# Optimization experiments

Hardware: AMD Instinct MI355X
Metric: run time of the kernel (lower is better)

Reference implementation:

```python
import jax, jax.numpy as jnp
import numpy as np

B, T, C = 2, 2048, 1024
NH = 16
DFF = 4096
EPS = 1e-5


def setup_inputs() -> dict:
    key = jax.random.key(0)
    ks = jax.random.split(key, 12)
    s = 0.02
    return {
        "x": jax.random.normal(ks[0], (B, T, C), dtype=jnp.float32),
        "Wq": jax.random.normal(ks[1], (C, C), dtype=jnp.float32) * s,
        "bq": jax.random.normal(ks[2], (C,), dtype=jnp.float32) * s,
        "Wk": jax.random.normal(ks[3], (C, C), dtype=jnp.float32) * s,
        "bk": jax.random.normal(ks[4], (C,), dtype=jnp.float32) * s,
        "Wv": jax.random.normal(ks[5], (C, C), dtype=jnp.float32) * s,
        "bv": jax.random.normal(ks[6], (C,), dtype=jnp.float32) * s,
        "W1": jax.random.normal(ks[7], (C, DFF), dtype=jnp.float32) * s,
        "b1": jax.random.normal(ks[8], (DFF,), dtype=jnp.float32) * s,
        "W2": jax.random.normal(ks[9], (DFF, C), dtype=jnp.float32) * s,
        "b2": jax.random.normal(ks[10], (C,), dtype=jnp.float32) * s,
        "ln_w": jnp.ones((C,), dtype=jnp.float32),
    }


def _layernorm(x, w):
    # LayerNorm over last dim, weight only (bias=False), eps=1e-5
    mu = jnp.mean(x, axis=-1, keepdims=True)
    var = jnp.mean(jnp.square(x - mu), axis=-1, keepdims=True)
    return (x - mu) / jnp.sqrt(var + EPS) * w


def reference(x, Wq, bq, Wk, bk, Wv, bv, W1, b1, W2, b2, ln_w):
    Bx, Tx, Cx = x.shape
    hd = Cx // NH
    q = (x @ Wq + bq).reshape(Bx, Tx, NH, hd).transpose(0, 2, 1, 3)  # [B,H,T,hd]
    k = (x @ Wk + bk).reshape(Bx, Tx, NH, hd).transpose(0, 2, 1, 3)
    v = (x @ Wv + bv).reshape(Bx, Tx, NH, hd).transpose(0, 2, 1, 3)
    # NOTE: original scales by sqrt(d_k) = sqrt(FULL model dim C), not head dim
    scores = jnp.einsum("bhqd,bhkd->bhqk", q, k) / jnp.sqrt(jnp.float32(Cx))
    causal = jnp.tril(jnp.ones((Tx, Tx), dtype=bool))
    scores = jnp.where(causal[None, None, :, :], scores, -jnp.inf)
    attn = jax.nn.softmax(scores, axis=-1)
    head_out = jnp.einsum("bhqk,bhkd->bhqd", attn, v)
    a = head_out.transpose(0, 2, 1, 3).reshape(Bx, Tx, Cx)
    # residuals: out = x + ln(x) with SHARED ln weight
    h = a + _layernorm(a, ln_w)
    f = jax.nn.relu(h @ W1 + b1) @ W2 + b2
    out = f + _layernorm(f, ln_w)
    return out
```

## Files before the change

kernel.cpp:

```cpp
#include <hip/hip_runtime.h>
#include <math.h>


typedef __attribute__((ext_vector_type(8))) short short8;
typedef __attribute__((ext_vector_type(4))) float f32x4;

__device__ __forceinline__ unsigned short f2bf(float f) {
    unsigned u = __builtin_bit_cast(unsigned, f);
    unsigned r = u + 0x7fffu + ((u >> 16) & 1u);
    return (unsigned short)(r >> 16);
}

__global__ __launch_bounds__(256) void prep_kernel(
    const float* __restrict__ x,  const float* __restrict__ Wq,
    const float* __restrict__ Wk, const float* __restrict__ Wv,
    const float* __restrict__ W1, const float* __restrict__ W2,
    const float* __restrict__ bq, const float* __restrict__ bk,
    unsigned short* __restrict__ x_bf,  unsigned short* __restrict__ Wqk_t,
    unsigned short* __restrict__ Wvt,   unsigned short* __restrict__ W1t,
    unsigned short* __restrict__ W2t,   float* __restrict__ bqk)
{
    const int bid = blockIdx.x;
    const int tid = threadIdx.x;

    if (bid < 4096) {
        const int i = (bid * 256 + tid) * 4;
        float4 v = *(const float4*)(x + i);
        ushort4 o;
        o.x = f2bf(v.x); o.y = f2bf(v.y); o.z = f2bf(v.z); o.w = f2bf(v.w);
        *(ushort4*)(x_bf + i) = o;
        return;
    }
    if (bid >= 6912) {
        const int i = (bid - 6912) * 256 + tid;
        bqk[i] = i < 1024 ? bq[i] : bk[i - 1024];
        return;
    }

    __shared__ float tile[64][65];
    const float* src; unsigned short* dst; int K, N, t;
    if (bid < 4352)      { t = bid - 4096; src = Wq; dst = Wqk_t;           K = 1024; N = 1024; }
    else if (bid < 4608) { t = bid - 4352; src = Wk; dst = Wqk_t + 1048576; K = 1024; N = 1024; }
    else if (bid < 4864) { t = bid - 4608; src = Wv; dst = Wvt;             K = 1024; N = 1024; }
    else if (bid < 5888) { t = bid - 4864; src = W1; dst = W1t;             K = 1024; N = 4096; }
    else                 { t = bid - 5888; src = W2; dst = W2t;             K = 4096; N = 1024; }

    const int ncols = N >> 6;
    const int n0 = (t % ncols) * 64;
    const int k0 = (t / ncols) * 64;
    const int tx = tid & 15;
    const int ty = tid >> 4;
#pragma unroll
    for (int i = 0; i < 4; ++i) {
        const int r = ty + i * 16;
        float4 v = *(const float4*)(src + (size_t)(k0 + r) * N + n0 + tx * 4);
        tile[r][tx * 4 + 0] = v.x;
        tile[r][tx * 4 + 1] = v.y;
        tile[r][tx * 4 + 2] = v.z;
        tile[r][tx * 4 + 3] = v.w;
    }
    __syncthreads();
#pragma unroll
    for (int i = 0; i < 4; ++i) {
        const int n = ty + i * 16;
        ushort4 o;
        o.x = f2bf(tile[tx * 4 + 0][n]);
        o.y = f2bf(tile[tx * 4 + 1][n]);
        o.z = f2bf(tile[tx * 4 + 2][n]);
        o.w = f2bf(tile[tx * 4 + 3][n]);
        *(ushort4*)(dst + (size_t)(n0 + n) * K + k0 + tx * 4) = o;
    }
}

template <int TM, int TN>
__device__ __forceinline__ void gemm_body(
    unsigned short* As, unsigned short* Bs,
    const unsigned short* __restrict__ A, const unsigned short* __restrict__ Bt,
    const float* __restrict__ bias, float* __restrict__ Cf,
    unsigned short* __restrict__ Cb, int M, int N, int K, int mode,
    int bx, int by, int kbeg, int kend)
{
    constexpr int NI   = TM / 32;
    constexpr int NJ   = TN / 32;
    constexpr int NPA  = TM / 8;
    constexpr int NPB  = TN / 8;
    constexpr int MAXA = (NPA + 3) / 4;
    constexpr int MAXB = (NPB + 3) / 4;

    const int tid  = threadIdx.x;
    const int lane = tid & 63;
    const int w    = tid >> 6;
    const int wm   = (w & 1) * (TM / 2);
    const int wn   = (w >> 1) * (TN / 2);
    const int fm   = lane & 15;
    const int quad = lane >> 4;

    const int row0 = by * TM;
    const int col0 = bx * TN;

    const int srow = lane >> 3;
    const int scol = ((lane & 7) ^ srow) << 3;

    const unsigned short* aptr[MAXA];
    int aoff[MAXA];
#pragma unroll
    for (int i = 0; i < MAXA; ++i) {
        const int p = w + i * 4;
        if (p < NPA) {
            aptr[i] = A + (size_t)(row0 + p * 8 + srow) * K + scol;
            aoff[i] = p * 8 * 64;
        }
    }
    const unsigned short* bptr[MAXB];
    int boff[MAXB];
#pragma unroll
    for (int i = 0; i < MAXB; ++i) {
        const int p = w + i * 4;
        if (p < NPB) {
            bptr[i] = Bt + (size_t)(col0 + p * 8 + srow) * K + scol;
            boff[i] = p * 8 * 64;
        }
    }

    f32x4 acc[NI][NJ] = {};

    for (int k0 = kbeg; k0 < kend; k0 += 64) {
        __syncthreads();
#pragma unroll
        for (int i = 0; i < MAXA; ++i)
            if (w + i * 4 < NPA)
                __builtin_amdgcn_global_load_lds(
                    (const __attribute__((address_space(1))) void*)(aptr[i] + k0),
                    (__attribute__((address_space(3))) void*)&As[aoff[i]], 16, 0, 0);
#pragma unroll
        for (int i = 0; i < MAXB; ++i)
            if (w + i * 4 < NPB)
                __builtin_amdgcn_global_load_lds(
                    (const __attribute__((address_space(1))) void*)(bptr[i] + k0),
                    (__attribute__((address_space(3))) void*)&Bs[boff[i]], 16, 0, 0);
        __syncthreads();

#pragma unroll
        for (int kh = 0; kh < 2; ++kh) {
            short8 af[NI], bf[NJ];
#pragma unroll
            for (int i = 0; i < NI; ++i) {
                const int r = wm + i * 16 + fm;
                const int sl = ((kh << 2) | quad) ^ (r & 7);
                af[i] = *(const short8*)&As[r * 64 + sl * 8];
            }
#pragma unroll
            for (int j = 0; j < NJ; ++j) {
                const int r = wn + j * 16 + fm;
                const int sl = ((kh << 2) | quad) ^ (r & 7);
                bf[j] = *(const short8*)&Bs[r * 64 + sl * 8];
            }
#pragma unroll
            for (int i = 0; i < NI; ++i)
#pragma unroll
                for (int j = 0; j < NJ; ++j)
                    acc[i][j] = __builtin_amdgcn_mfma_f32_16x16x32_bf16(
                        af[i], bf[j], acc[i][j], 0, 0, 0);
        }
    }

#pragma unroll
    for (int j = 0; j < NJ; ++j) {
        const int col = col0 + wn + j * 16 + fm;
        const float bcol = (mode == 3 || mode == 4) ? 0.f : bias[col];
#pragma unroll
        for (int i = 0; i < NI; ++i) {
            const int rbase = row0 + wm + i * 16 + quad * 4;
#pragma unroll
            for (int r = 0; r < 4; ++r) {
                const int row = rbase + r;
                float val = acc[i][j][r] + ((mode == 3) ? bias[row] : bcol);
                if (mode == 1) val = fmaxf(val, 0.f);
                if (mode == 0 || mode == 4) Cf[(size_t)row * N + col] = val;
                else                        Cb[(size_t)row * N + col] = f2bf(val);
            }
        }
    }
}

template <int TM, int TN>
__global__ __launch_bounds__(256) void gemm_bf16_mfma(
    const unsigned short* __restrict__ A, const unsigned short* __restrict__ Bt,
    const float* __restrict__ bias, float* __restrict__ Cf,
    unsigned short* __restrict__ Cb, int M, int N, int K, int mode)
{
    __shared__ unsigned short As[TM * 64];
    __shared__ unsigned short Bs[TN * 64];
    gemm_body<TM, TN>(As, Bs, A, Bt, bias, Cf, Cb, M, N, K, mode,
                      blockIdx.x, blockIdx.y, 0, K);
}

template <int TM, int TN>
__global__ __launch_bounds__(256) void gemm_splitk(
    const unsigned short* __restrict__ A, const unsigned short* __restrict__ Bt,
    const float* __restrict__ bias, float* __restrict__ C0,
    float* __restrict__ C1, int M, int N, int K,
    int nxh, int rows_per_xcd_h, int nbh)
{
    __shared__ unsigned short As[TM * 64];
    __shared__ unsigned short Bs[TN * 64];
    const int half = blockIdx.x >= nbh;
    const int r    = blockIdx.x - (half ? nbh : 0);
    const int xcd  = blockIdx.x & 7;
    const int idx  = r >> 3;
    const int bx   = idx % nxh;
    const int by   = xcd * rows_per_xcd_h + idx / nxh;
    const int kb   = half ? (K >> 1) : 0;
    gemm_body<TM, TN>(As, Bs, A, Bt, bias, half ? C1 : C0, nullptr,
                      M, N, K, half ? 4 : 0, bx, by, kb, kb + (K >> 1));
}

template <int TM, int TN>
__global__ __launch_bounds__(256) void gemm_dual(
    const unsigned short* __restrict__ A0, const unsigned short* __restrict__ B0,
    const float* __restrict__ bias0, unsigned short* __restrict__ C0,
    int M0, int N0, int K0, int mode0, int nb0, int nx0,
    const unsigned short* __restrict__ A1, const unsigned short* __restrict__ B1,
    const float* __restrict__ bias1, unsigned short* __restrict__ C1,
    int M1, int N1, int K1, int mode1, int nx1)
{
    __shared__ unsigned short As[TM * 64];
    __shared__ unsigned short Bs[TN * 64];
    const int bid = blockIdx.x;
    if (bid < nb0) {
        gemm_body<TM, TN>(As, Bs, A0, B0, bias0, nullptr, C0,
                          M0, N0, K0, mode0, bid % nx0, bid / nx0, 0, K0);
    } else {
        const int t = bid - nb0;
        gemm_body<TM, TN>(As, Bs, A1, B1, bias1, nullptr, C1,
                          M1, N1, K1, mode1, t % nx1, t / nx1, 0, K1);
    }
}

__global__ __launch_bounds__(256) void fattn_mfma(
    const unsigned short* __restrict__ qk,
    const unsigned short* __restrict__ vt,
    float* __restrict__ a)
{
    const int T = 2048, LDQK = 2048, LDVT = 4096, OUTC = 1024;
    const float cs = 0.04508422f;

    __shared__ unsigned short Qs[64 * 64];
    __shared__ unsigned short Ks[64 * 64];
    __shared__ unsigned short Vs[64 * 64];
    __shared__ unsigned short Ps[4][16][72];

    const int tid  = threadIdx.x;
    const int lane = tid & 63;
    const int w    = tid >> 6;
    const int fm   = lane & 15;
    const int quad = lane >> 4;
    const int srow = lane >> 3;
    const int scol = ((lane & 7) ^ srow) << 3;

    const int n  = blockIdx.x;
    const int lo = n & 255, hi = n >> 8;
    const int h  = ((lo >> 5) & 7) | ((hi & 1) << 3);
    const int b  = hi >> 1;
    const int qv = lo & 31;
    const int u  = ((qv & 1) << 4) | ((qv & 2) << 2) | (qv & 4) |
                   ((qv & 8) >> 2) | ((qv & 16) >> 4);
    const int qb = (hi & 1) ? (31 - u) : u;
    const int q0 = qb * 64;

    const size_t rowbase = (size_t)b * T;

#pragma unroll
    for (int i = 0; i < 2; ++i) {
        const int p = w * 2 + i;
        const unsigned short* src = qk + (rowbase + q0 + p * 8 + srow) * LDQK
                                       + h * 64 + scol;
        __builtin_amdgcn_global_load_lds(
            (const __attribute__((address_space(1))) void*)src,
            (__attribute__((address_space(3))) void*)&Qs[p * 8 * 64], 16, 0, 0);
    }
    __syncthreads();
    const int qr = w * 16 + fm;
    short8 qf0 = *(const short8*)&Qs[qr * 64 + ((quad ^ (qr & 7)) << 3)];
    short8 qf1 = *(const short8*)&Qs[qr * 64 + (((4 | quad) ^ (qr & 7)) << 3)];

    short8 ones;
#pragma unroll
    for (int i = 0; i < 8; ++i) ones[i] = (short)0x3F80;

    f32x4 o[4] = {};
    f32x4 lacc = {};

    const int qglob = q0 + w * 16 + fm;

    for (int jt = 0; jt <= qb; ++jt) {
        const int j0 = jt * 64;
        __syncthreads();
#pragma unroll
        for (int i = 0; i < 4; ++i) {
            const int unit = w * 4 + i;
            if (unit < 8) {
                const unsigned short* ksrc = qk + (rowbase + j0 + unit * 8 + srow) * LDQK
                                                + 1024 + h * 64 + scol;
                __builtin_amdgcn_global_load_lds(
                    (const __attribute__((address_space(1))) void*)ksrc,
                    (__attribute__((address_space(3))) void*)&Ks[unit * 8 * 64], 16, 0, 0);
            } else {
                const int p = unit - 8;
                const unsigned short* vsrc = vt + (size_t)(h * 64 + p * 8 + srow) * LDVT
                                                + rowbase + j0 + scol;
                __builtin_amdgcn_global_load_lds(
                    (const __attribute__((address_space(1))) void*)vsrc,
                    (__attribute__((address_space(3))) void*)&Vs[p * 8 * 64], 16, 0, 0);
            }
        }
        __syncthreads();

        f32x4 s[4];
#pragma unroll
        for (int j = 0; j < 4; ++j) {
            const int r = j * 16 + fm;
            short8 k0 = *(const short8*)&Ks[r * 64 + ((quad ^ (r & 7)) << 3)];
            short8 k1 = *(const short8*)&Ks[r * 64 + (((4 | quad) ^ (r & 7)) << 3)];
            f32x4 acc = {};
            acc = __builtin_amdgcn_mfma_f32_16x16x32_bf16(k0, qf0, acc, 0, 0, 0);
            acc = __builtin_amdgcn_mfma_f32_16x16x32_bf16(k1, qf1, acc, 0, 0, 0);
            s[j] = acc;
        }

        if (jt == qb) {
#pragma unroll
            for (int j = 0; j < 4; ++j) {
                const int kbase = j0 + j * 16 + quad * 4;
#pragma unroll
                for (int r = 0; r < 4; ++r) {
                    const float e = exp2f(s[j][r] * cs);
                    s[j][r] = (kbase + r > qglob) ? 0.f : e;
                }
            }
        } else {
#pragma unroll
            for (int j = 0; j < 4; ++j)
#pragma unroll
                for (int r = 0; r < 4; ++r)
                    s[j][r] = exp2f(s[j][r] * cs);
        }

#pragma unroll
        for (int j = 0; j < 4; ++j) {
            unsigned d0, d1;
            asm("v_cvt_pk_bf16_f32 %0, %1, %2"
                : "=v"(d0) : "v"(s[j][0]), "v"(s[j][1]));
            asm("v_cvt_pk_bf16_f32 %0, %1, %2"
                : "=v"(d1) : "v"(s[j][2]), "v"(s[j][3]));
            *(uint2*)&Ps[w][fm][j * 16 + quad * 4] = make_uint2(d0, d1);
        }
        short8 pf0 = *(const short8*)&Ps[w][fm][quad * 8];
        short8 pf1 = *(const short8*)&Ps[w][fm][32 + quad * 8];

#pragma unroll
        for (int jd = 0; jd < 4; ++jd) {
            const int r = jd * 16 + fm;
            short8 v0 = *(const short8*)&Vs[r * 64 + ((quad ^ (r & 7)) << 3)];
            short8 v1 = *(const short8*)&Vs[r * 64 + (((4 | quad) ^ (r & 7)) << 3)];
            o[jd] = __builtin_amdgcn_mfma_f32_16x16x32_bf16(pf0, v0, o[jd], 0, 0, 0);
            o[jd] = __builtin_amdgcn_mfma_f32_16x16x32_bf16(pf1, v1, o[jd], 0, 0, 0);
        }
        lacc = __builtin_amdgcn_mfma_f32_16x16x32_bf16(pf0, ones, lacc, 0, 0, 0);
        lacc = __builtin_amdgcn_mfma_f32_16x16x32_bf16(pf1, ones, lacc, 0, 0, 0);
    }

    const size_t orow = rowbase + q0 + w * 16 + quad * 4;
#pragma unroll
    for (int r = 0; r < 4; ++r) {
        const float inv = 1.0f / lacc[r];
#pragma unroll
        for (int jd = 0; jd < 4; ++jd)
            a[(orow + r) * OUTC + h * 64 + jd * 16 + fm] = o[jd][r] * inv;
    }
}

__global__ __launch_bounds__(256) void add_ln_kernel(
    const float* __restrict__ in, const float* __restrict__ in2,
    const float* __restrict__ w,
    float* __restrict__ outf, unsigned short* __restrict__ outb, int bf16_out)
{
    const int C = 1024;
    const int row = blockIdx.x;
    const int tid = threadIdx.x;
    const int lane = tid & 63;
    const int wv   = tid >> 6;

    __shared__ float red[8];

    float4 xv = *(const float4*)(in + (size_t)row * C + tid * 4);
    if (in2) {
        float4 yv = *(const float4*)(in2 + (size_t)row * C + tid * 4);
        xv.x += yv.x; xv.y += yv.y; xv.z += yv.z; xv.w += yv.w;
    }

    float s = xv.x + xv.y + xv.z + xv.w;
#pragma unroll
    for (int o = 32; o > 0; o >>= 1) s += __shfl_xor(s, o, 64);
    if (lane == 0) red[wv] = s;
    __syncthreads();
    const float mu = (red[0] + red[1] + red[2] + red[3]) * (1.0f / 1024.0f);

    float dx = xv.x - mu, dy = xv.y - mu, dz = xv.z - mu, dw = xv.w - mu;
    float v = dx * dx + dy * dy + dz * dz + dw * dw;
#pragma unroll
    for (int o = 32; o > 0; o >>= 1) v += __shfl_xor(v, o, 64);
    if (lane == 0) red[4 + wv] = v;
    __syncthreads();
    const float rstd = rsqrtf((red[4] + red[5] + red[6] + red[7]) * (1.0f / 1024.0f)
                              + 1e-5f);

    float4 wvv = *(const float4*)(w + tid * 4);
    float ox = xv.x + dx * rstd * wvv.x;
    float oy = xv.y + dy * rstd * wvv.y;
    float oz = xv.z + dz * rstd * wvv.z;
    float ow = xv.w + dw * rstd * wvv.w;
    if (bf16_out) {
        ushort4 o4;
        o4.x = f2bf(ox); o4.y = f2bf(oy); o4.z = f2bf(oz); o4.w = f2bf(ow);
        *(ushort4*)(outb + (size_t)row * C + tid * 4) = o4;
    } else {
        *(float4*)(outf + (size_t)row * C + tid * 4) = make_float4(ox, oy, oz, ow);
    }
}

extern "C" void kernel_launch(void* const* d_in, const int* in_sizes, int n_in,
                              void* d_out, int out_size, void* d_ws, size_t ws_size,
                              hipStream_t stream)
{
    const float* x    = (const float*)d_in[0];
    const float* Wq   = (const float*)d_in[1];
    const float* bq   = (const float*)d_in[2];
    const float* Wk   = (const float*)d_in[3];
    const float* bk   = (const float*)d_in[4];
    const float* Wv   = (const float*)d_in[5];
    const float* bv   = (const float*)d_in[6];
    const float* W1   = (const float*)d_in[7];
    const float* b1   = (const float*)d_in[8];
    const float* W2   = (const float*)d_in[9];
    const float* b2   = (const float*)d_in[10];
    const float* ln_w = (const float*)d_in[11];
    float* out = (float*)d_out;
    char* ws = (char*)d_ws;

    const int B = 2, T = 2048, C = 1024, DFF = 4096;
    const int M = B * T;
    const size_t MB = 1048576;

    unsigned short* qk_bf = (unsigned short*)(ws);
    unsigned short* vt_bf = (unsigned short*)(ws + 16 * MB);
    float*          a     = (float*)(ws + 24 * MB);
    unsigned short* x_bf  = (unsigned short*)(ws + 40 * MB);
    unsigned short* Wqk_t = (unsigned short*)(ws + 48 * MB);
    unsigned short* Wvt   = (unsigned short*)(ws + 52 * MB);
    unsigned short* W1t   = (unsigned short*)(ws + 54 * MB);
    unsigned short* W2t   = (unsigned short*)(ws + 62 * MB);
    float*          bqk   = (float*)(ws + 70 * MB);
    unsigned short* u_bf  = (unsigned short*)(ws + 71 * MB);
    unsigned short* h_bf  = x_bf;
    float*          f     = (float*)(ws);
    float*          f2    = a;

    dim3 blk(256);

    prep_kernel<<<dim3(6920), blk, 0, stream>>>(
        x, Wq, Wk, Wv, W1, W2, bq, bk,
        x_bf, Wqk_t, Wvt, W1t, W2t, bqk);

    gemm_dual<64, 128><<<dim3(1536), blk, 0, stream>>>(
        x_bf, Wqk_t, bqk, qk_bf, M, 2 * C, C, 2, 1024, 16,
        Wvt, x_bf, bv, vt_bf, C, M, C, 3, 32);

    fattn_mfma<<<dim3(1024), blk, 0, stream>>>(qk_bf, vt_bf, a);

    add_ln_kernel<<<dim3(M), blk, 0, stream>>>(a, nullptr, ln_w, nullptr, h_bf, 1);

    gemm_bf16_mfma<64, 128><<<dim3(DFF / 128, M / 64), blk, 0, stream>>>(
        h_bf, W1t, b1, nullptr, u_bf, M, DFF, C, 1);

    gemm_splitk<128, 64><<<dim3(1024), blk, 0, stream>>>(
        u_bf, W2t, b2, f, f2, M, C, DFF, 16, 4, 512);

    add_ln_kernel<<<dim3(M), blk, 0, stream>>>(f, f2, ln_w, out, nullptr, 0);
}
```

Measured before the change: 313.2 us.

## Process two adjacent query tiles per attention block to reuse K/V loads

Each attention workgroup now handles two consecutive 64-row query tiles, sharing every K/V tile loaded into LDS between them. This roughly halves K/V global traffic and barrier count per unit of work, and halves the grid to 512 blocks with a new head/batch/pair index mapping. In exchange it adds register pressure (two sets of accumulators and Q fragments), uses more LDS, and gives fewer blocks for load balancing across CUs.

Measured after the change: 331.9 us. 6.0% more time.

```diff
diff --git a/kernel.cpp b/kernel.cpp
--- a/kernel.cpp
+++ b/kernel.cpp
@@ -245,7 +245,7 @@
     const int T = 2048, LDQK = 2048, LDVT = 4096, OUTC = 1024;
     const float cs = 0.04508422f;
 
-    __shared__ unsigned short Qs[64 * 64];
+    __shared__ unsigned short Qs[2][64 * 64];
     __shared__ unsigned short Ks[64 * 64];
     __shared__ unsigned short Vs[64 * 64];
     __shared__ unsigned short Ps[4][16][72];
@@ -259,41 +259,101 @@
     const int scol = ((lane & 7) ^ srow) << 3;
 
     const int n  = blockIdx.x;
-    const int lo = n & 255, hi = n >> 8;
-    const int h  = ((lo >> 5) & 7) | ((hi & 1) << 3);
-    const int b  = hi >> 1;
-    const int qv = lo & 31;
-    const int u  = ((qv & 1) << 4) | ((qv & 2) << 2) | (qv & 4) |
-                   ((qv & 8) >> 2) | ((qv & 16) >> 4);
-    const int qb = (hi & 1) ? (31 - u) : u;
-    const int q0 = qb * 64;
+    const int p4 = n & 15;
+    const int h  = (n >> 4) & 15;
+    const int b  = n >> 8;
+    const int u  = ((p4 & 1) << 3) | ((p4 & 2) << 1) |
+                   ((p4 & 4) >> 1) | ((p4 & 8) >> 3);
+    const int p  = b ? (15 - u) : u;
+    const int ta = 2 * p, tb = 2 * p + 1;
+    const int q0a = ta * 64;
 
     const size_t rowbase = (size_t)b * T;
 
 #pragma unroll
-    for (int i = 0; i < 2; ++i) {
-        const int p = w * 2 + i;
-        const unsigned short* src = qk + (rowbase + q0 + p * 8 + srow) * LDQK
+    for (int i = 0; i < 8; ++i) {
+        const int unit = w * 8 + i;
+        const int tile = unit >> 4, pan = unit & 15;
+        const unsigned short* src = qk + (rowbase + q0a + tile * 64 + pan * 8 + srow) * LDQK
                                        + h * 64 + scol;
         __builtin_amdgcn_global_load_lds(
             (const __attribute__((address_space(1))) void*)src,
-            (__attribute__((address_space(3))) void*)&Qs[p * 8 * 64], 16, 0, 0);
+            (__attribute__((address_space(3))) void*)&Qs[tile][pan * 8 * 64], 16, 0, 0);
     }
     __syncthreads();
     const int qr = w * 16 + fm;
-    short8 qf0 = *(const short8*)&Qs[qr * 64 + ((quad ^ (qr & 7)) << 3)];
-    short8 qf1 = *(const short8*)&Qs[qr * 64 + (((4 | quad) ^ (qr & 7)) << 3)];
+    short8 qa0 = *(const short8*)&Qs[0][qr * 64 + ((quad ^ (qr & 7)) << 3)];
+    short8 qa1 = *(const short8*)&Qs[0][qr * 64 + (((4 | quad) ^ (qr & 7)) << 3)];
+    short8 qbf0 = *(const short8*)&Qs[1][qr * 64 + ((quad ^ (qr & 7)) << 3)];
+    short8 qbf1 = *(const short8*)&Qs[1][qr * 64 + (((4 | quad) ^ (qr & 7)) << 3)];
 
     short8 ones;
 #pragma unroll
     for (int i = 0; i < 8; ++i) ones[i] = (short)0x3F80;
 
-    f32x4 o[4] = {};
-    f32x4 lacc = {};
-
-    const int qglob = q0 + w * 16 + fm;
-
-    for (int jt = 0; jt <= qb; ++jt) {
+    f32x4 oA[4] = {}, oB[4] = {};
+    f32x4 laccA = {}, laccB = {};
+
+    const int qglobA = q0a + w * 16 + fm;
+    const int qglobB = q0a + 64 + w * 16 + fm;
+
+    auto process = [&](short8 qf0, short8 qf1, int qglob, int masked,
+                       f32x4* o, f32x4& lacc, int j0) {
+        f32x4 s[4];
+#pragma unroll
+        for (int j = 0; j < 4; ++j) {
+            const int r = j * 16 + fm;
+            short8 k0 = *(const short8*)&Ks[r * 64 + ((quad ^ (r & 7)) << 3)];
+            short8 k1 = *(const short8*)&Ks[r * 64 + (((4 | quad) ^ (r & 7)) << 3)];
+            f32x4 acc = {};
+            acc = __builtin_amdgcn_mfma_f32_16x16x32_bf16(k0, qf0, acc, 0, 0, 0);
+            acc = __builtin_amdgcn_mfma_f32_16x16x32_bf16(k1, qf1, acc, 0, 0, 0);
+            s[j] = acc;
+        }
+
+        if (masked) {
+#pragma unroll
+            for (int j = 0; j < 4; ++j) {
+                const int kbase = j0 + j * 16 + quad * 4;
+#pragma unroll
+                for (int r = 0; r < 4; ++r) {
+                    const float e = exp2f(s[j][r] * cs);
+                    s[j][r] = (kbase + r > qglob) ? 0.f : e;
+                }
+            }
+        } else {
+#pragma unroll
+            for (int j = 0; j < 4; ++j)
+#pragma unroll
+                for (int r = 0; r < 4; ++r)
+                    s[j][r] = exp2f(s[j][r] * cs);
+        }
+
+#pragma unroll
+        for (int j = 0; j < 4; ++j) {
+            unsigned d0, d1;
+            asm("v_cvt_pk_bf16_f32 %0, %1, %2"
+                : "=v"(d0) : "v"(s[j][0]), "v"(s[j][1]));
+            asm("v_cvt_pk_bf16_f32 %0, %1, %2"
+                : "=v"(d1) : "v"(s[j][2]), "v"(s[j][3]));
+            *(uint2*)&Ps[w][fm][j * 16 + quad * 4] = make_uint2(d0, d1);
+        }
+        short8 pf0 = *(const short8*)&Ps[w][fm][quad * 8];
+        short8 pf1 = *(const short8*)&Ps[w][fm][32 + quad * 8];
+
+#pragma unroll
+        for (int jd = 0; jd < 4; ++jd) {
+            const int r = jd * 16 + fm;
+            short8 v0 = *(const short8*)&Vs[r * 64 + ((quad ^ (r & 7)) << 3)];
+            short8 v1 = *(const short8*)&Vs[r * 64 + (((4 | quad) ^ (r & 7)) << 3)];
+            o[jd] = __builtin_amdgcn_mfma_f32_16x16x32_bf16(pf0, v0, o[jd], 0, 0, 0);
+            o[jd] = __builtin_amdgcn_mfma_f32_16x16x32_bf16(pf1, v1, o[jd], 0, 0, 0);
+        }
+        lacc = __builtin_amdgcn_mfma_f32_16x16x32_bf16(pf0, ones, lacc, 0, 0, 0);
+        lacc = __builtin_amdgcn_mfma_f32_16x16x32_bf16(pf1, ones, lacc, 0, 0, 0);
+    };
+
+    for (int jt = 0; jt <= tb; ++jt) {
         const int j0 = jt * 64;
         __syncthreads();
 #pragma unroll
@@ -306,77 +366,32 @@
                     (const __attribute__((address_space(1))) void*)ksrc,
                     (__attribute__((address_space(3))) void*)&Ks[unit * 8 * 64], 16, 0, 0);
             } else {
-                const int p = unit - 8;
-                const unsigned short* vsrc = vt + (size_t)(h * 64 + p * 8 + srow) * LDVT
+                const int pn = unit - 8;
+                const unsigned short* vsrc = vt + (size_t)(h * 64 + pn * 8 + srow) * LDVT
                                                 + rowbase + j0 + scol;
                 __builtin_amdgcn_global_load_lds(
                     (const __attribute__((address_space(1))) void*)vsrc,
-                    (__attribute__((address_space(3))) void*)&Vs[p * 8 * 64], 16, 0, 0);
+                    (__attribute__((address_space(3))) void*)&Vs[pn * 8 * 64], 16, 0, 0);
             }
         }
         __syncthreads();
 
-        f32x4 s[4];
-#pragma unroll
-        for (int j = 0; j < 4; ++j) {
-            const int r = j * 16 + fm;
-            short8 k0 = *(const short8*)&Ks[r * 64 + ((quad ^ (r & 7)) << 3)];
-            short8 k1 = *(const short8*)&Ks[r * 64 + (((4 | quad) ^ (r & 7)) << 3)];
-            f32x4 acc = {};
-            acc = __builtin_amdgcn_mfma_f32_16x16x32_bf16(k0, qf0, acc, 0, 0, 0);
-            acc = __builtin_amdgcn_mfma_f32_16x16x32_bf16(k1, qf1, acc, 0, 0, 0);
-            s[j] = acc;
-        }
-
-        if (jt == qb) {
-#pragma unroll
-            for (int j = 0; j < 4; ++j) {
-                const int kbase = j0 + j * 16 + quad * 4;
-#pragma unroll
-                for (int r = 0; r < 4; ++r) {
-                    const float e = exp2f(s[j][r] * cs);
-                    s[j][r] = (kbase + r > qglob) ? 0.f : e;
-                }
-            }
-        } else {
-#pragma unroll
-            for (int j = 0; j < 4; ++j)
-#pragma unroll
-                for (int r = 0; r < 4; ++r)
-                    s[j][r] = exp2f(s[j][r] * cs);
-        }
-
-#pragma unroll
-        for (int j = 0; j < 4; ++j) {
-            unsigned d0, d1;
-            asm("v_cvt_pk_bf16_f32 %0, %1, %2"
-                : "=v"(d0) : "v"(s[j][0]), "v"(s[j][1]));
-            asm("v_cvt_pk_bf16_f32 %0, %1, %2"
-                : "=v"(d1) : "v"(s[j][2]), "v"(s[j][3]));
-            *(uint2*)&Ps[w][fm][j * 16 + quad * 4] = make_uint2(d0, d1);
-        }
-        short8 pf0 = *(const short8*)&Ps[w][fm][quad * 8];
-        short8 pf1 = *(const short8*)&Ps[w][fm][32 + quad * 8];
-
+        if (jt <= ta)
+            process(qa0, qa1, qglobA, jt == ta, oA, laccA, j0);
+        process(qbf0, qbf1, qglobB, jt == tb, oB, laccB, j0);
+    }
+
+    const size_t orA = rowbase + q0a + w * 16 + quad * 4;
+    const size_t orB = orA + 64;
+#pragma unroll
+    for (int r = 0; r < 4; ++r) {
+        const float invA = 1.0f / laccA[r];
+        const float invB = 1.0f / laccB[r];
 #pragma unroll
         for (int jd = 0; jd < 4; ++jd) {
-            const int r = jd * 16 + fm;
-            short8 v0 = *(const short8*)&Vs[r * 64 + ((quad ^ (r & 7)) << 3)];
-            short8 v1 = *(const short8*)&Vs[r * 64 + (((4 | quad) ^ (r & 7)) << 3)];
-            o[jd] = __builtin_amdgcn_mfma_f32_16x16x32_bf16(pf0, v0, o[jd], 0, 0, 0);
-            o[jd] = __builtin_amdgcn_mfma_f32_16x16x32_bf16(pf1, v1, o[jd], 0, 0, 0);
-        }
-        lacc = __builtin_amdgcn_mfma_f32_16x16x32_bf16(pf0, ones, lacc, 0, 0, 0);
-        lacc = __builtin_amdgcn_mfma_f32_16x16x32_bf16(pf1, ones, lacc, 0, 0, 0);
-    }
-
-    const size_t orow = rowbase + q0 + w * 16 + quad * 4;
-#pragma unroll
-    for (int r = 0; r < 4; ++r) {
-        const float inv = 1.0f / lacc[r];
-#pragma unroll
-        for (int jd = 0; jd < 4; ++jd)
-            a[(orow + r) * OUTC + h * 64 + jd * 16 + fm] = o[jd][r] * inv;
+            a[(orA + r) * OUTC + h * 64 + jd * 16 + fm] = oA[jd][r] * invA;
+            a[(orB + r) * OUTC + h * 64 + jd * 16 + fm] = oB[jd][r] * invB;
+        }
     }
 }
 
@@ -476,7 +491,7 @@
         x_bf, Wqk_t, bqk, qk_bf, M, 2 * C, C, 2, 1024, 16,
         Wvt, x_bf, bv, vt_bf, C, M, C, 3, 32);
 
-    fattn_mfma<<<dim3(1024), blk, 0, stream>>>(qk_bf, vt_bf, a);
+    fattn_mfma<<<dim3(512), blk, 0, stream>>>(qk_bf, vt_bf, a);
 
     add_ln_kernel<<<dim3(M), blk, 0, stream>>>(a, nullptr, ln_w, nullptr, h_bf, 1);
 
```

## Double-buffer GEMM LDS tiles to overlap global loads with MFMA compute

Applied to the files above, without the earlier changes.

The GEMM body now keeps two LDS buffers per operand and issues the global_load_lds for the next K tile before computing on the current one. It waits with a partial vmcnt so only the current tile's loads must have landed, and uses raw s_barrier in place of __syncthreads. The goal is to hide global memory latency behind MFMA work, at the cost of twice the LDS footprint, which may lower occupancy. Correctness depends on the vmcnt count matching the per-wave load count and on the LDS DMA ordering.

Result: slower. 339.8 us (+8.5%).

```diff
diff --git a/kernel.cpp b/kernel.cpp
--- a/kernel.cpp
+++ b/kernel.cpp
@@ -86,6 +86,9 @@
     constexpr int NPB  = TN / 8;
     constexpr int MAXA = (NPA + 3) / 4;
     constexpr int MAXB = (NPB + 3) / 4;
+    constexpr int ASZ  = TM * 64;
+    constexpr int BSZ  = TN * 64;
+    constexpr int LPW  = (NPA + NPB) / 4;
 
     const int tid  = threadIdx.x;
     const int lane = tid & 63;
@@ -122,23 +125,38 @@
         }
     }
 
-    f32x4 acc[NI][NJ] = {};
-
-    for (int k0 = kbeg; k0 < kend; k0 += 64) {
-        __syncthreads();
+    auto stage = [&](int k0, unsigned short* Ab, unsigned short* Bb) {
 #pragma unroll
         for (int i = 0; i < MAXA; ++i)
             if (w + i * 4 < NPA)
                 __builtin_amdgcn_global_load_lds(
                     (const __attribute__((address_space(1))) void*)(aptr[i] + k0),
-                    (__attribute__((address_space(3))) void*)&As[aoff[i]], 16, 0, 0);
+                    (__attribute__((address_space(3))) void*)&Ab[aoff[i]], 16, 0, 0);
 #pragma unroll
         for (int i = 0; i < MAXB; ++i)
             if (w + i * 4 < NPB)
                 __builtin_amdgcn_global_load_lds(
                     (const __attribute__((address_space(1))) void*)(bptr[i] + k0),
-                    (__attribute__((address_space(3))) void*)&Bs[boff[i]], 16, 0, 0);
-        __syncthreads();
+                    (__attribute__((address_space(3))) void*)&Bb[boff[i]], 16, 0, 0);
+    };
+
+    f32x4 acc[NI][NJ] = {};
+
+    stage(kbeg, As, Bs);
+    const int NT = (kend - kbeg) >> 6;
+
+    for (int t = 0; t < NT; ++t) {
+        unsigned short* Ac = As + (t & 1) * ASZ;
+        unsigned short* Bc = Bs + (t & 1) * BSZ;
+
+        if (t + 1 < NT) {
+            stage(kbeg + (t + 1) * 64, As + ((t + 1) & 1) * ASZ,
+                                       Bs + ((t + 1) & 1) * BSZ);
+            asm volatile("s_waitcnt vmcnt(%0)" :: "n"(LPW) : "memory");
+        } else {
+            asm volatile("s_waitcnt vmcnt(0)" ::: "memory");
+        }
+        __builtin_amdgcn_s_barrier();
 
 #pragma unroll
         for (int kh = 0; kh < 2; ++kh) {
@@ -147,13 +165,13 @@
             for (int i = 0; i < NI; ++i) {
                 const int r = wm + i * 16 + fm;
                 const int sl = ((kh << 2) | quad) ^ (r & 7);
-                af[i] = *(const short8*)&As[r * 64 + sl * 8];
+                af[i] = *(const short8*)&Ac[r * 64 + sl * 8];
             }
 #pragma unroll
             for (int j = 0; j < NJ; ++j) {
                 const int r = wn + j * 16 + fm;
                 const int sl = ((kh << 2) | quad) ^ (r & 7);
-                bf[j] = *(const short8*)&Bs[r * 64 + sl * 8];
+                bf[j] = *(const short8*)&Bc[r * 64 + sl * 8];
             }
 #pragma unroll
             for (int i = 0; i < NI; ++i)
@@ -162,6 +180,8 @@
                     acc[i][j] = __builtin_amdgcn_mfma_f32_16x16x32_bf16(
                         af[i], bf[j], acc[i][j], 0, 0, 0);
         }
+
+        __builtin_amdgcn_s_barrier();
     }
 
 #pragma unroll
@@ -189,8 +209,8 @@
     const float* __restrict__ bias, float* __restrict__ Cf,
     unsigned short* __restrict__ Cb, int M, int N, int K, int mode)
 {
-    __shared__ unsigned short As[TM * 64];
-    __shared__ unsigned short Bs[TN * 64];
+    __shared__ unsigned short As[2 * TM * 64];
+    __shared__ unsigned short Bs[2 * TN * 64];
     gemm_body<TM, TN>(As, Bs, A, Bt, bias, Cf, Cb, M, N, K, mode,
                       blockIdx.x, blockIdx.y, 0, K);
 }
@@ -202,8 +222,8 @@
     float* __restrict__ C1, int M, int N, int K,
     int nxh, int rows_per_xcd_h, int nbh)
 {
-    __shared__ unsigned short As[TM * 64];
-    __shared__ unsigned short Bs[TN * 64];
+    __shared__ unsigned short As[2 * TM * 64];
+    __shared__ unsigned short Bs[2 * TN * 64];
     const int half = blockIdx.x >= nbh;
     const int r    = blockIdx.x - (half ? nbh : 0);
     const int xcd  = blockIdx.x & 7;
@@ -224,8 +244,8 @@
     const float* __restrict__ bias1, unsigned short* __restrict__ C1,
     int M1, int N1, int K1, int mode1, int nx1)
 {
-    __shared__ unsigned short As[TM * 64];
-    __shared__ unsigned short Bs[TN * 64];
+    __shared__ unsigned short As[2 * TM * 64];
+    __shared__ unsigned short Bs[2 * TN * 64];
     const int bid = blockIdx.x;
     if (bid < nb0) {
         gemm_body<TM, TN>(As, Bs, A0, B0, bias0, nullptr, C0,
```
